# Optimization experiments

Hardware: AMD Instinct MI355X
Metric: run time of the kernel (lower is better)

## Reference

```python
import jax, jax.numpy as jnp
import numpy as np

N, IN_DIM, OUT_DIM, HEADS = 8192, 256, 128, 2


def setup_inputs() -> dict:
    key = jax.random.key(0)
    k1, k2, k3, k4, k5 = jax.random.split(key, 5)
    features = jax.random.normal(k1, (N, IN_DIM), dtype=jnp.float32)
    adjacency = jax.random.randint(k2, (N, N), 0, 2, dtype=jnp.int32)
    # nn.Linear(input_dim, output_dim*heads, bias=False): weight [out, in]
    W = jax.random.normal(k3, (OUT_DIM * HEADS, IN_DIM), dtype=jnp.float32) * 0.05
    attn_src = jax.random.normal(k4, (HEADS, OUT_DIM), dtype=jnp.float32) * 0.05
    attn_dst = jax.random.normal(k5, (HEADS, OUT_DIM), dtype=jnp.float32) * 0.05
    return {"features": features, "adjacency": adjacency, "W": W,
            "attn_src": attn_src, "attn_dst": attn_dst}


def reference(features, adjacency, W, attn_src, attn_dst):
    n = features.shape[0]
    # transformed: [N, H, F]
    transformed = (features @ W.T).reshape(n, HEADS, OUT_DIM)
    src_scores = jnp.einsum('nhf,hf->nh', transformed, attn_src)  # [N, H]
    dst_scores = jnp.einsum('nhf,hf->nh', transformed, attn_dst)  # [N, H]
    # logits: [N_src, N_dst, H]
    logits = jax.nn.leaky_relu(src_scores[:, None, :] + dst_scores[None, :, :],
                               negative_slope=0.2)
    mask = adjacency > 0  # [N, N]
    logits = jnp.where(mask[:, :, None], logits, -jnp.inf)
    attention = jax.nn.softmax(logits, axis=1)  # softmax over dst dim (dim=1)
    attention = jnp.nan_to_num(attention, nan=0.0, posinf=0.0, neginf=0.0)
    aggregated = jnp.einsum('ijh,jhf->ihf', attention, transformed)  # [N, H, F]
    return aggregated.mean(axis=1)  # [N, F]
```

## Files before the change

### kernel.cpp

```cpp
#include <hip/hip_runtime.h>
#include <stdint.h>
#include <stddef.h>

#define NN 8192
#define KD 256
#define CD 256
#define FD 128
#define BI 32
#define BJ 32
#define PACK_BLOCKS 1024

typedef __attribute__((ext_vector_type(4))) float f32x4;
typedef __attribute__((ext_vector_type(8))) short b16x8;

__device__ __forceinline__ unsigned short f2bf(float x) {
    unsigned int u = __float_as_uint(x);
    u += 0x7fffu + ((u >> 16) & 1u);
    return (unsigned short)(u >> 16);
}

__device__ __forceinline__ void async16(const void* g, void* l) {
    __builtin_amdgcn_global_load_lds(
        (const __attribute__((address_space(1))) unsigned int*)g,
        (__attribute__((address_space(3))) unsigned int*)l, 16, 0, 0);
}

__device__ __forceinline__ float exp_pack_store(
    int m8, const float4 d0, const float4 d1, float sv, unsigned short* wdst)
{
    const float dd[8] = {d0.x, d0.y, d0.z, d0.w, d1.x, d1.y, d1.z, d1.w};
    const float ninf = __int_as_float(0xff800000);
    float e[8]; float dp = 0.f;
#pragma unroll
    for (int k = 0; k < 8; ++k) {
        float x = sv + dd[k];
        x = fmaxf(x, 0.f) + 0.2f * fminf(x, 0.f);
        x = (m8 & (1 << k)) ? x : ninf;
        const float ev = __expf(x);
        dp += ev; e[k] = ev;
    }
    union { unsigned short us[8]; b16x8 v; } pk;
#if __has_builtin(__builtin_amdgcn_cvt_pk_bf16_f32)
#pragma unroll
    for (int k = 0; k < 4; ++k) {
        auto p = __builtin_amdgcn_cvt_pk_bf16_f32(e[2 * k], e[2 * k + 1]);
        __builtin_memcpy(&pk.us[2 * k], &p, 4);
    }
#else
#pragma unroll
    for (int k = 0; k < 8; ++k) pk.us[k] = f2bf(e[k]);
#endif
    *(b16x8*)wdst = pk.v;
    return dp;
}

__global__ __launch_bounds__(256) void k_front(
    const float* __restrict__ feat, const float* __restrict__ W,
    const float* __restrict__ asrc, const float* __restrict__ adst,
    const int* __restrict__ adj, unsigned int* __restrict__ mask,
    unsigned short* __restrict__ Tt, float* __restrict__ s_t, float* __restrict__ d_t)
{
    __shared__ unsigned short a_lds[64 * 32];
    __shared__ unsigned short b_lds[256 * 32];
    __shared__ unsigned short tr_lds[256 * 72];
    __shared__ float sc_lds[4][64];
    __shared__ float dc_lds[4][64];

    const int t = threadIdx.x;

    if (blockIdx.x >= 128) {
        const int pb = blockIdx.x - 128;
        const size_t base = (size_t)pb * 16384;
        const int4* a4 = (const int4*)adj;
#pragma unroll 4
        for (int st = 0; st < 64; ++st) {
            const size_t i4 = base + (size_t)st * 256 + t;
            const int4 v = a4[i4];
            unsigned int nib = (v.x != 0 ? 1u : 0u) | (v.y != 0 ? 2u : 0u) |
                               (v.z != 0 ? 4u : 0u) | (v.w != 0 ? 8u : 0u);
            unsigned int wd = nib << (4 * (t & 7));
            wd |= __shfl_xor(wd, 1);
            wd |= __shfl_xor(wd, 2);
            wd |= __shfl_xor(wd, 4);
            if ((t & 7) == 0) mask[i4 >> 3] = wd;
        }
        return;
    }

    const int wave = t >> 6, lane = t & 63;
    const int l15 = lane & 15, quad = lane >> 4;
    const int n0 = blockIdx.x * 64;
    const int ai = t >> 2, ag = t & 3;

    f32x4 acc[4][4] = {};
    for (int kc = 0; kc < 8; ++kc) {
        const int k0 = kc * 32;
        __syncthreads();
        {
            const float* src = feat + (size_t)(n0 + ai) * KD + k0 + ag * 8;
            const float4 v0 = *(const float4*)src;
            const float4 v1 = *(const float4*)(src + 4);
            union { unsigned short us[8]; b16x8 v; } pk;
            pk.us[0] = f2bf(v0.x); pk.us[1] = f2bf(v0.y);
            pk.us[2] = f2bf(v0.z); pk.us[3] = f2bf(v0.w);
            pk.us[4] = f2bf(v1.x); pk.us[5] = f2bf(v1.y);
            pk.us[6] = f2bf(v1.z); pk.us[7] = f2bf(v1.w);
            const int slot = ag ^ ((ai >> 1) & 3);
            *(b16x8*)&a_lds[ai * 32 + slot * 8] = pk.v;
        }
        for (int p = 0; p < 4; ++p) {
            const int G = p * 256 + t;
            const int c = G >> 2, g = G & 3;
            const float* src = W + (size_t)c * KD + k0 + g * 8;
            const float4 v0 = *(const float4*)src;
            const float4 v1 = *(const float4*)(src + 4);
            union { unsigned short us[8]; b16x8 v; } pk;
            pk.us[0] = f2bf(v0.x); pk.us[1] = f2bf(v0.y);
            pk.us[2] = f2bf(v0.z); pk.us[3] = f2bf(v0.w);
            pk.us[4] = f2bf(v1.x); pk.us[5] = f2bf(v1.y);
            pk.us[6] = f2bf(v1.z); pk.us[7] = f2bf(v1.w);
            const int slot = g ^ ((c >> 1) & 3);
            *(b16x8*)&b_lds[c * 32 + slot * 8] = pk.v;
        }
        __syncthreads();
        b16x8 af[4], bfr[4];
        for (int mt = 0; mt < 4; ++mt) {
            const int m = mt * 16 + l15;
            af[mt] = *(const b16x8*)&a_lds[m * 32 + (quad ^ ((m >> 1) & 3)) * 8];
        }
        for (int nt = 0; nt < 4; ++nt) {
            const int c = wave * 64 + nt * 16 + l15;
            bfr[nt] = *(const b16x8*)&b_lds[c * 32 + (quad ^ ((c >> 1) & 3)) * 8];
        }
        for (int mt = 0; mt < 4; ++mt)
            for (int nt = 0; nt < 4; ++nt)
                acc[mt][nt] = __builtin_amdgcn_mfma_f32_16x16x32_bf16(
                    af[mt], bfr[nt], acc[mt][nt], 0, 0, 0);
    }

    float aS[4], aD[4];
    for (int nt = 0; nt < 4; ++nt) {
        const int c = wave * 64 + nt * 16 + l15;
        aS[nt] = asrc[c]; aD[nt] = adst[c];
    }
    for (int mt = 0; mt < 4; ++mt)
        for (int r = 0; r < 4; ++r) {
            float vs = 0.f, vd = 0.f;
            for (int nt = 0; nt < 4; ++nt) {
                const float x = acc[mt][nt][r];
                vs += x * aS[nt]; vd += x * aD[nt];
            }
            vs += __shfl_xor(vs, 1); vd += __shfl_xor(vd, 1);
            vs += __shfl_xor(vs, 2); vd += __shfl_xor(vd, 2);
            vs += __shfl_xor(vs, 4); vd += __shfl_xor(vd, 4);
            vs += __shfl_xor(vs, 8); vd += __shfl_xor(vd, 8);
            if (l15 == 0) {
                const int nl = mt * 16 + quad * 4 + r;
                sc_lds[wave][nl] = vs; dc_lds[wave][nl] = vd;
            }
        }
    for (int mt = 0; mt < 4; ++mt)
        for (int nt = 0; nt < 4; ++nt)
            for (int r = 0; r < 4; ++r) {
                const int c = wave * 64 + nt * 16 + l15;
                const int n = mt * 16 + quad * 4 + r;
                tr_lds[c * 72 + n] = f2bf(acc[mt][nt][r]);
            }
    __syncthreads();
    if (t < 128) {
        const int n = t >> 1, h = t & 1;
        s_t[(size_t)h * NN + n0 + n] = sc_lds[h * 2][n] + sc_lds[h * 2 + 1][n];
        d_t[(size_t)h * NN + n0 + n] = dc_lds[h * 2][n] + dc_lds[h * 2 + 1][n];
    }
    for (int p = 0; p < 8; ++p) {
        const int idx = p * 256 + t;
        const int c = idx >> 3, g = idx & 7;
        *(b16x8*)(Tt + (size_t)c * NN + n0 + g * 8) = *(const b16x8*)&tr_lds[c * 72 + g * 8];
    }
}

__global__ __launch_bounds__(256, 4) void k_gat(
    const unsigned char* __restrict__ maskb, const unsigned short* __restrict__ Tt,
    const float* __restrict__ s_t, const float* __restrict__ d_t,
    float* __restrict__ num_part,
    float* __restrict__ den_part,
    int njt)
{
    __shared__ unsigned short tt_lds[2][256 * 32];
    __shared__ unsigned short w_lds[2][2][32][32];

    const int t = threadIdx.x;
    const int wave = t >> 6, lane = t & 63;
    const int l15 = lane & 15, quad = lane >> 4;
    const int i0 = blockIdx.x * BI;
    const int chunk = blockIdx.y;
    const size_t jbase = (size_t)chunk * njt * BJ;

    const int eh = t >> 7;
    const int wi = (t & 127) >> 2;
    const int g4 = t & 3;
    const int gi = i0 + wi;
    const float sv = s_t[(size_t)eh * NN + gi];
    const int wslot = (g4 ^ ((wi >> 1) & 3)) * 8;

    const int mh = wave >> 1, fh = wave & 1;
    const int cbase = mh * 128 + fh * 64;

    f32x4 acc[2][4] = {};
    float den = 0.f;

    const unsigned char* mrow = maskb + (size_t)gi * (NN / 8) + (jbase >> 3) + g4;
    const float* dp_ = d_t + (size_t)eh * NN + jbase + g4 * 8;

    for (int p = 0; p < 4; ++p) {
        const int G = (p * 4 + wave) * 64 + lane;
        const int c = G >> 2;
        const int g = (G & 3) ^ ((c >> 1) & 3);
        async16(Tt + (size_t)c * NN + jbase + g * 8,
                (char*)&tt_lds[0][0] + (size_t)(p * 4 + wave) * 1024);
    }
    __builtin_amdgcn_sched_barrier(0);
    int cM = mrow[0];
    float4 cD0 = ((const float4*)dp_)[0], cD1 = ((const float4*)dp_)[1];
    {
        const int j1 = (njt > 1) ? 1 : 0;
        int nM = mrow[j1 * 4];
        float4 nD0 = *(const float4*)(dp_ + j1 * BJ);
        float4 nD1 = *(const float4*)(dp_ + j1 * BJ + 4);
        den += exp_pack_store(cM, cD0, cD1, sv, &w_lds[0][eh][wi][wslot]);
        cM = nM; cD0 = nD0; cD1 = nD1;
    }
    asm volatile("s_waitcnt vmcnt(3) lgkmcnt(0)\n\ts_barrier" ::: "memory");

    for (int jt = 0; jt < njt; ++jt) {
        const int cur = jt & 1, nxt = cur ^ 1;
        b16x8 af[2], bfr[4];
        for (int mt = 0; mt < 2; ++mt) {
            const int m = mt * 16 + l15;
            af[mt] = *(const b16x8*)&w_lds[cur][mh][m][(quad ^ ((m >> 1) & 3)) * 8];
        }
        for (int nt = 0; nt < 4; ++nt) {
            const int c = cbase + nt * 16 + l15;
            bfr[nt] = *(const b16x8*)&tt_lds[cur][c * 32 + (quad ^ ((c >> 1) & 3)) * 8];
        }
        const size_t jnext = jbase + (size_t)((jt + 1 < njt) ? jt + 1 : jt) * BJ;
        for (int p = 0; p < 4; ++p) {
            const int G = (p * 4 + wave) * 64 + lane;
            const int c = G >> 2;
            const int g = (G & 3) ^ ((c >> 1) & 3);
            async16(Tt + (size_t)c * NN + jnext + g * 8,
                    (char*)&tt_lds[nxt][0] + (size_t)(p * 4 + wave) * 1024);
        }
        __builtin_amdgcn_sched_barrier(0);
        const int j2 = ((jt + 2 < njt) ? jt + 2 : njt - 1);
        int nM = mrow[j2 * 4];
        float4 nD0 = *(const float4*)(dp_ + j2 * BJ);
        float4 nD1 = *(const float4*)(dp_ + j2 * BJ + 4);
        const float dpv = exp_pack_store(cM, cD0, cD1, sv,
                                         &w_lds[nxt][eh][wi][wslot]);
        if (jt + 1 < njt) den += dpv;
        for (int mt = 0; mt < 2; ++mt)
            for (int nt = 0; nt < 4; ++nt)
                acc[mt][nt] = __builtin_amdgcn_mfma_f32_16x16x32_bf16(
                    af[mt], bfr[nt], acc[mt][nt], 0, 0, 0);
        cM = nM; cD0 = nD0; cD1 = nD1;
        asm volatile("s_waitcnt vmcnt(3) lgkmcnt(0)\n\ts_barrier" ::: "memory");
    }

    float dv = den;
    dv += __shfl_xor(dv, 1); dv += __shfl_xor(dv, 2);
    if (g4 == 0)
        den_part[((size_t)chunk * 2 + eh) * NN + gi] = dv;

    float* np_ = num_part + (size_t)chunk * NN * CD;
    for (int mt = 0; mt < 2; ++mt)
        for (int nt = 0; nt < 4; ++nt)
            for (int r = 0; r < 4; ++r) {
                const int n = i0 + mt * 16 + quad * 4 + r;
                const int c = cbase + nt * 16 + l15;
                np_[(size_t)n * CD + c] = acc[mt][nt][r];
            }
}

__global__ __launch_bounds__(256) void k_combine(
    const float* __restrict__ num_part, const float* __restrict__ den_part,
    float* __restrict__ out, int jsplit)
{
    const int idx = blockIdx.x * 256 + threadIdx.x;
    const int n = idx >> 7, f = idx & 127;
    const size_t row = (size_t)n * CD;
    float n0 = 0.f, n1 = 0.f, d0 = 0.f, d1 = 0.f;
    for (int c = 0; c < jsplit; ++c) {
        const size_t base = (size_t)c * NN * CD;
        n0 += num_part[base + row + f];
        n1 += num_part[base + row + 128 + f];
        d0 += den_part[((size_t)c * 2 + 0) * NN + n];
        d1 += den_part[((size_t)c * 2 + 1) * NN + n];
    }
    const float r0 = d0 != 0.f ? n0 / d0 : 0.f;
    const float r1 = d1 != 0.f ? n1 / d1 : 0.f;
    out[idx] = 0.5f * (r0 + r1);
}

extern "C" void kernel_launch(void* const* d_in, const int* in_sizes, int n_in,
                              void* d_out, int out_size, void* d_ws, size_t ws_size,
                              hipStream_t stream) {
    const float* feat = (const float*)d_in[0];
    const int*   adj  = (const int*)d_in[1];
    const float* W    = (const float*)d_in[2];
    const float* asrc = (const float*)d_in[3];
    const float* adst = (const float*)d_in[4];
    float* out = (float*)d_out;

    const int jsplit = (ws_size >= ((size_t)45 << 20)) ? 4 : 2;
    const int njt = (NN / jsplit) / BJ;

    char* ws = (char*)d_ws;
    unsigned short* Tt = (unsigned short*)ws;
    float* s_t  = (float*)(ws + ((size_t)4 << 20));
    float* d_t  = (float*)(ws + ((size_t)4 << 20) + (64 << 10));
    float* den  = (float*)(ws + ((size_t)4 << 20) + (128 << 10));
    unsigned int* mask = (unsigned int*)(ws + ((size_t)5 << 20));
    float* nump = (float*)(ws + ((size_t)13 << 20));

    k_front<<<128 + PACK_BLOCKS, 256, 0, stream>>>(feat, W, asrc, adst, adj,
                                                   mask, Tt, s_t, d_t);
    k_gat<<<dim3(NN / BI, jsplit), 256, 0, stream>>>((const unsigned char*)mask,
                                                     Tt, s_t, d_t, nump, den, njt);
    k_combine<<<NN * FD / 256, 256, 0, stream>>>(nump, den, out, jsplit);
}
```

Before: 506.2 us.

## Drop LDS staging in GAT kernel; compute attention fragments directly in registers

The GAT aggregation kernel no longer stages the transformed features and attention weights through double-buffered LDS. Each wave now handles one head and 32 rows, computes its exp/bf16 attention fragment straight into MFMA A-operand registers, and loads the B fragments directly from global memory. Block tile grows to 64 rows, with per-wave accumulators doubled to 2x8 tiles and occupancy hint lowered to 3. This removes LDS traffic and barriers, but gives up software prefetch. Each global load of Tt is also shared by fewer rows per wave, so more global and L2 traffic is expected.

```diff
diff --git a/kernel.cpp b/kernel.cpp
--- a/kernel.cpp
+++ b/kernel.cpp
@@ -6,8 +6,6 @@
 #define KD 256
 #define CD 256
 #define FD 128
-#define BI 32
-#define BJ 32
 #define PACK_BLOCKS 1024
 
 typedef __attribute__((ext_vector_type(4))) float f32x4;
@@ -19,14 +17,8 @@
     return (unsigned short)(u >> 16);
 }
 
-__device__ __forceinline__ void async16(const void* g, void* l) {
-    __builtin_amdgcn_global_load_lds(
-        (const __attribute__((address_space(1))) unsigned int*)g,
-        (__attribute__((address_space(3))) unsigned int*)l, 16, 0, 0);
-}
-
-__device__ __forceinline__ float exp_pack_store(
-    int m8, const float4 d0, const float4 d1, float sv, unsigned short* wdst)
+__device__ __forceinline__ float exp_frag(
+    int m8, const float4 d0, const float4 d1, float sv, b16x8* frag)
 {
     const float dd[8] = {d0.x, d0.y, d0.z, d0.w, d1.x, d1.y, d1.z, d1.w};
     const float ninf = __int_as_float(0xff800000);
@@ -50,7 +42,7 @@
 #pragma unroll
     for (int k = 0; k < 8; ++k) pk.us[k] = f2bf(e[k]);
 #endif
-    *(b16x8*)wdst = pk.v;
+    *frag = pk.v;
     return dp;
 }
 
@@ -179,105 +171,73 @@
     }
 }
 
-__global__ __launch_bounds__(256, 4) void k_gat(
+__global__ __launch_bounds__(256, 3) void k_gat(
     const unsigned char* __restrict__ maskb, const unsigned short* __restrict__ Tt,
     const float* __restrict__ s_t, const float* __restrict__ d_t,
     float* __restrict__ num_part,
     float* __restrict__ den_part,
     int njt)
 {
-    __shared__ unsigned short tt_lds[2][256 * 32];
-    __shared__ unsigned short w_lds[2][2][32][32];
-
     const int t = threadIdx.x;
     const int wave = t >> 6, lane = t & 63;
     const int l15 = lane & 15, quad = lane >> 4;
-    const int i0 = blockIdx.x * BI;
+    const int h = wave >> 1, ih = wave & 1;
+    const int i0 = blockIdx.x * 64 + ih * 32;
     const int chunk = blockIdx.y;
-    const size_t jbase = (size_t)chunk * njt * BJ;
-
-    const int eh = t >> 7;
-    const int wi = (t & 127) >> 2;
-    const int g4 = t & 3;
-    const int gi = i0 + wi;
-    const float sv = s_t[(size_t)eh * NN + gi];
-    const int wslot = (g4 ^ ((wi >> 1) & 3)) * 8;
-
-    const int mh = wave >> 1, fh = wave & 1;
-    const int cbase = mh * 128 + fh * 64;
-
-    f32x4 acc[2][4] = {};
-    float den = 0.f;
-
-    const unsigned char* mrow = maskb + (size_t)gi * (NN / 8) + (jbase >> 3) + g4;
-    const float* dp_ = d_t + (size_t)eh * NN + jbase + g4 * 8;
-
-    for (int p = 0; p < 4; ++p) {
-        const int G = (p * 4 + wave) * 64 + lane;
-        const int c = G >> 2;
-        const int g = (G & 3) ^ ((c >> 1) & 3);
-        async16(Tt + (size_t)c * NN + jbase + g * 8,
-                (char*)&tt_lds[0][0] + (size_t)(p * 4 + wave) * 1024);
-    }
-    __builtin_amdgcn_sched_barrier(0);
-    int cM = mrow[0];
-    float4 cD0 = ((const float4*)dp_)[0], cD1 = ((const float4*)dp_)[1];
-    {
-        const int j1 = (njt > 1) ? 1 : 0;
-        int nM = mrow[j1 * 4];
-        float4 nD0 = *(const float4*)(dp_ + j1 * BJ);
-        float4 nD1 = *(const float4*)(dp_ + j1 * BJ + 4);
-        den += exp_pack_store(cM, cD0, cD1, sv, &w_lds[0][eh][wi][wslot]);
-        cM = nM; cD0 = nD0; cD1 = nD1;
-    }
-    asm volatile("s_waitcnt vmcnt(3) lgkmcnt(0)\n\ts_barrier" ::: "memory");
+    const size_t jbase = (size_t)chunk * njt * 32;
+
+    const int r0 = i0 + l15;
+    const int r1 = i0 + 16 + l15;
+    const float sv0 = s_t[(size_t)h * NN + r0];
+    const float sv1 = s_t[(size_t)h * NN + r1];
+
+    const unsigned char* m0 = maskb + (size_t)r0 * (NN / 8) + (jbase >> 3) + quad;
+    const unsigned char* m1 = maskb + (size_t)r1 * (NN / 8) + (jbase >> 3) + quad;
+    const float* dp = d_t + (size_t)h * NN + jbase + quad * 8;
+    const unsigned short* tb = Tt + (size_t)(h * 128 + l15) * NN + jbase + quad * 8;
+
+    f32x4 acc[2][8] = {};
+    float den0 = 0.f, den1 = 0.f;
 
     for (int jt = 0; jt < njt; ++jt) {
-        const int cur = jt & 1, nxt = cur ^ 1;
-        b16x8 af[2], bfr[4];
-        for (int mt = 0; mt < 2; ++mt) {
-            const int m = mt * 16 + l15;
-            af[mt] = *(const b16x8*)&w_lds[cur][mh][m][(quad ^ ((m >> 1) & 3)) * 8];
-        }
-        for (int nt = 0; nt < 4; ++nt) {
-            const int c = cbase + nt * 16 + l15;
-            bfr[nt] = *(const b16x8*)&tt_lds[cur][c * 32 + (quad ^ ((c >> 1) & 3)) * 8];
-        }
-        const size_t jnext = jbase + (size_t)((jt + 1 < njt) ? jt + 1 : jt) * BJ;
-        for (int p = 0; p < 4; ++p) {
-            const int G = (p * 4 + wave) * 64 + lane;
-            const int c = G >> 2;
-            const int g = (G & 3) ^ ((c >> 1) & 3);
-            async16(Tt + (size_t)c * NN + jnext + g * 8,
-                    (char*)&tt_lds[nxt][0] + (size_t)(p * 4 + wave) * 1024);
-        }
-        __builtin_amdgcn_sched_barrier(0);
-        const int j2 = ((jt + 2 < njt) ? jt + 2 : njt - 1);
-        int nM = mrow[j2 * 4];
-        float4 nD0 = *(const float4*)(dp_ + j2 * BJ);
-        float4 nD1 = *(const float4*)(dp_ + j2 * BJ + 4);
-        const float dpv = exp_pack_store(cM, cD0, cD1, sv,
-                                         &w_lds[nxt][eh][wi][wslot]);
-        if (jt + 1 < njt) den += dpv;
-        for (int mt = 0; mt < 2; ++mt)
-            for (int nt = 0; nt < 4; ++nt)
-                acc[mt][nt] = __builtin_amdgcn_mfma_f32_16x16x32_bf16(
-                    af[mt], bfr[nt], acc[mt][nt], 0, 0, 0);
-        cM = nM; cD0 = nD0; cD1 = nD1;
-        asm volatile("s_waitcnt vmcnt(3) lgkmcnt(0)\n\ts_barrier" ::: "memory");
-    }
-
-    float dv = den;
-    dv += __shfl_xor(dv, 1); dv += __shfl_xor(dv, 2);
-    if (g4 == 0)
-        den_part[((size_t)chunk * 2 + eh) * NN + gi] = dv;
+        const int jo = jt * 32;
+        const int mb0 = m0[jt * 4];
+        const int mb1 = m1[jt * 4];
+        const float4 dv0 = *(const float4*)(dp + jo);
+        const float4 dv1 = *(const float4*)(dp + jo + 4);
+        b16x8 bfr[8];
+#pragma unroll
+        for (int nt = 0; nt < 8; ++nt)
+            bfr[nt] = *(const b16x8*)(tb + (size_t)nt * 16 * NN + jo);
+        b16x8 a0, a1;
+        den0 += exp_frag(mb0, dv0, dv1, sv0, &a0);
+        den1 += exp_frag(mb1, dv0, dv1, sv1, &a1);
+#pragma unroll
+        for (int nt = 0; nt < 8; ++nt)
+            acc[0][nt] = __builtin_amdgcn_mfma_f32_16x16x32_bf16(
+                a0, bfr[nt], acc[0][nt], 0, 0, 0);
+#pragma unroll
+        for (int nt = 0; nt < 8; ++nt)
+            acc[1][nt] = __builtin_amdgcn_mfma_f32_16x16x32_bf16(
+                a1, bfr[nt], acc[1][nt], 0, 0, 0);
+    }
+
+    den0 += __shfl_xor(den0, 16); den0 += __shfl_xor(den0, 32);
+    den1 += __shfl_xor(den1, 16); den1 += __shfl_xor(den1, 32);
+    if (quad == 0) {
+        den_part[((size_t)chunk * 2 + h) * NN + r0] = den0;
+        den_part[((size_t)chunk * 2 + h) * NN + r1] = den1;
+    }
 
     float* np_ = num_part + (size_t)chunk * NN * CD;
+#pragma unroll
     for (int mt = 0; mt < 2; ++mt)
-        for (int nt = 0; nt < 4; ++nt)
+#pragma unroll
+        for (int nt = 0; nt < 8; ++nt)
+#pragma unroll
             for (int r = 0; r < 4; ++r) {
                 const int n = i0 + mt * 16 + quad * 4 + r;
-                const int c = cbase + nt * 16 + l15;
+                const int c = h * 128 + nt * 16 + l15;
                 np_[(size_t)n * CD + c] = acc[mt][nt][r];
             }
 }
@@ -313,7 +273,7 @@
     float* out = (float*)d_out;
 
     const int jsplit = (ws_size >= ((size_t)45 << 20)) ? 4 : 2;
-    const int njt = (NN / jsplit) / BJ;
+    const int njt = (NN / jsplit) / 32;
 
     char* ws = (char*)d_ws;
     unsigned short* Tt = (unsigned short*)ws;
@@ -325,7 +285,7 @@
 
     k_front<<<128 + PACK_BLOCKS, 256, 0, stream>>>(feat, W, asrc, adst, adj,
                                                    mask, Tt, s_t, d_t);
-    k_gat<<<dim3(NN / BI, jsplit), 256, 0, stream>>>((const unsigned char*)mask,
+    k_gat<<<dim3(NN / 64, jsplit), 256, 0, stream>>>((const unsigned char*)mask,
                                                      Tt, s_t, d_t, nump, den, njt);
     k_combine<<<NN * FD / 256, 256, 0, stream>>>(nump, den, out, jsplit);
 }
```

Measured after the change: 565.8 us. +11.8%, slower.

## Factor exp of leaky-relu into precomputed per-node exponentials and tile mask/T layouts

Applied to the files above, without the earlier changes.

Replaces the per-edge exp(leaky_relu(s+d)) with max(exp(s)exp(d), exp(0.2s)exp(0.2d)), using four per-node exponential arrays computed in the front kernel. This removes the transcendental from the inner loop, leaving two multiplies and a max per edge. The mask is repacked into a 32-row tiled transposed layout and the transformed features into contiguous 32-column blocks, so each tile load hits one contiguous region. Skipping max-subtraction risks overflow for large scores, and the inner loop now issues more global loads per tile.

```diff
diff --git a/kernel.cpp b/kernel.cpp
--- a/kernel.cpp
+++ b/kernel.cpp
@@ -8,7 +8,7 @@
 #define FD 128
 #define BI 32
 #define BJ 32
-#define PACK_BLOCKS 1024
+#define PACK_BLOCKS 512
 
 typedef __attribute__((ext_vector_type(4))) float f32x4;
 typedef __attribute__((ext_vector_type(8))) short b16x8;
@@ -25,19 +25,18 @@
         (__attribute__((address_space(3))) unsigned int*)l, 16, 0, 0);
 }
 
-__device__ __forceinline__ float exp_pack_store(
-    int m8, const float4 d0, const float4 d1, float sv, unsigned short* wdst)
+__device__ __forceinline__ float wsel_store(
+    int m8, const float4 f0, const float4 f1, const float4 h0, const float4 h1,
+    float Ei, float Gi, unsigned short* wdst)
 {
-    const float dd[8] = {d0.x, d0.y, d0.z, d0.w, d1.x, d1.y, d1.z, d1.w};
-    const float ninf = __int_as_float(0xff800000);
+    const float ff[8] = {f0.x, f0.y, f0.z, f0.w, f1.x, f1.y, f1.z, f1.w};
+    const float hh[8] = {h0.x, h0.y, h0.z, h0.w, h1.x, h1.y, h1.z, h1.w};
     float e[8]; float dp = 0.f;
 #pragma unroll
     for (int k = 0; k < 8; ++k) {
-        float x = sv + dd[k];
-        x = fmaxf(x, 0.f) + 0.2f * fminf(x, 0.f);
-        x = (m8 & (1 << k)) ? x : ninf;
-        const float ev = __expf(x);
-        dp += ev; e[k] = ev;
+        float w = fmaxf(Ei * ff[k], Gi * hh[k]);
+        w = (m8 & (1 << k)) ? w : 0.f;
+        dp += w; e[k] = w;
     }
     union { unsigned short us[8]; b16x8 v; } pk;
 #if __has_builtin(__builtin_amdgcn_cvt_pk_bf16_f32)
@@ -57,32 +56,44 @@
 __global__ __launch_bounds__(256) void k_front(
     const float* __restrict__ feat, const float* __restrict__ W,
     const float* __restrict__ asrc, const float* __restrict__ adst,
-    const int* __restrict__ adj, unsigned int* __restrict__ mask,
-    unsigned short* __restrict__ Tt, float* __restrict__ s_t, float* __restrict__ d_t)
+    const int* __restrict__ adj, unsigned char* __restrict__ MT,
+    unsigned short* __restrict__ TB,
+    float* __restrict__ SE, float* __restrict__ SG,
+    float* __restrict__ SF, float* __restrict__ SH)
 {
     __shared__ unsigned short a_lds[64 * 32];
     __shared__ unsigned short b_lds[256 * 32];
     __shared__ unsigned short tr_lds[256 * 72];
     __shared__ float sc_lds[4][64];
     __shared__ float dc_lds[4][64];
+    __shared__ unsigned char pk_lds[1024 * 16];
 
     const int t = threadIdx.x;
 
     if (blockIdx.x >= 128) {
         const int pb = blockIdx.x - 128;
-        const size_t base = (size_t)pb * 16384;
+        const int I = pb >> 1, half = pb & 1;
+        const int row_base = I * 32 + half * 16;
         const int4* a4 = (const int4*)adj;
 #pragma unroll 4
-        for (int st = 0; st < 64; ++st) {
-            const size_t i4 = base + (size_t)st * 256 + t;
-            const int4 v = a4[i4];
+        for (int st = 0; st < 128; ++st) {
+            const int g = st * 256 + t;
+            const int row16 = g >> 11;
+            const int j4 = g & 2047;
+            const int4 v = a4[(size_t)(row_base + row16) * 2048 + j4];
             unsigned int nib = (v.x != 0 ? 1u : 0u) | (v.y != 0 ? 2u : 0u) |
                                (v.z != 0 ? 4u : 0u) | (v.w != 0 ? 8u : 0u);
-            unsigned int wd = nib << (4 * (t & 7));
-            wd |= __shfl_xor(wd, 1);
-            wd |= __shfl_xor(wd, 2);
-            wd |= __shfl_xor(wd, 4);
-            if ((t & 7) == 0) mask[i4 >> 3] = wd;
+            unsigned int b = nib << (4 * (t & 1));
+            b |= __shfl_xor(b, 1);
+            if ((t & 1) == 0) pk_lds[(j4 >> 1) * 16 + row16] = (unsigned char)b;
+        }
+        __syncthreads();
+        unsigned int* mt32 = (unsigned int*)MT;
+        const unsigned int* src = (const unsigned int*)pk_lds;
+        for (int i = 0; i < 16; ++i) {
+            const int w = i * 256 + t;
+            const int jb = w >> 2, r4 = w & 3;
+            mt32[(size_t)I * 8192 + jb * 8 + half * 4 + r4] = src[w];
         }
         return;
     }
@@ -169,19 +180,26 @@
     __syncthreads();
     if (t < 128) {
         const int n = t >> 1, h = t & 1;
-        s_t[(size_t)h * NN + n0 + n] = sc_lds[h * 2][n] + sc_lds[h * 2 + 1][n];
-        d_t[(size_t)h * NN + n0 + n] = dc_lds[h * 2][n] + dc_lds[h * 2 + 1][n];
+        const float s = sc_lds[h * 2][n] + sc_lds[h * 2 + 1][n];
+        const float d = dc_lds[h * 2][n] + dc_lds[h * 2 + 1][n];
+        SE[(size_t)h * NN + n0 + n] = __expf(s);
+        SG[(size_t)h * NN + n0 + n] = __expf(0.2f * s);
+        SF[(size_t)h * NN + n0 + n] = __expf(d);
+        SH[(size_t)h * NN + n0 + n] = __expf(0.2f * d);
     }
     for (int p = 0; p < 8; ++p) {
         const int idx = p * 256 + t;
         const int c = idx >> 3, g = idx & 7;
-        *(b16x8*)(Tt + (size_t)c * NN + n0 + g * 8) = *(const b16x8*)&tr_lds[c * 72 + g * 8];
+        unsigned short* dst = TB + ((size_t)((n0 >> 5) + (g >> 2))) * 8192
+                              + c * 32 + (g & 3) * 8;
+        *(b16x8*)dst = *(const b16x8*)&tr_lds[c * 72 + g * 8];
     }
 }
 
 __global__ __launch_bounds__(256, 4) void k_gat(
-    const unsigned char* __restrict__ maskb, const unsigned short* __restrict__ Tt,
-    const float* __restrict__ s_t, const float* __restrict__ d_t,
+    const unsigned char* __restrict__ MT, const unsigned short* __restrict__ TB,
+    const float* __restrict__ SE, const float* __restrict__ SG,
+    const float* __restrict__ SF, const float* __restrict__ SH,
     float* __restrict__ num_part,
     float* __restrict__ den_part,
     int njt)
@@ -197,74 +215,81 @@
     const size_t jbase = (size_t)chunk * njt * BJ;
 
     const int eh = t >> 7;
-    const int wi = (t & 127) >> 2;
+    const int wi = (t >> 2) & 31;
     const int g4 = t & 3;
     const int gi = i0 + wi;
-    const float sv = s_t[(size_t)eh * NN + gi];
-    const int wslot = (g4 ^ ((wi >> 1) & 3)) * 8;
+    const float Ei = SE[(size_t)eh * NN + gi];
+    const float Gi = SG[(size_t)eh * NN + gi];
+    const int wslot = (g4 ^ (wi & 3) ^ ((wi >> 2) & 3)) * 8;
 
     const int mh = wave >> 1, fh = wave & 1;
-    const int cbase = mh * 128 + fh * 64;
+    const int cb = mh * 128 + fh * 64;
 
     f32x4 acc[2][4] = {};
     float den = 0.f;
 
-    const unsigned char* mrow = maskb + (size_t)gi * (NN / 8) + (jbase >> 3) + g4;
-    const float* dp_ = d_t + (size_t)eh * NN + jbase + g4 * 8;
+    const unsigned short* tb0 = TB + (jbase >> 5) * 8192;
+    const unsigned char* mrow = MT + ((size_t)(i0 >> 5)) * 32768
+                                + (jbase >> 3) * 32 + g4 * 32 + wi;
+    const float* fp = SF + (size_t)eh * NN + jbase + g4 * 8;
+    const float* hp = SH + (size_t)eh * NN + jbase + g4 * 8;
 
     for (int p = 0; p < 4; ++p) {
         const int G = (p * 4 + wave) * 64 + lane;
         const int c = G >> 2;
         const int g = (G & 3) ^ ((c >> 1) & 3);
-        async16(Tt + (size_t)c * NN + jbase + g * 8,
+        async16(tb0 + (size_t)c * 32 + g * 8,
                 (char*)&tt_lds[0][0] + (size_t)(p * 4 + wave) * 1024);
     }
     __builtin_amdgcn_sched_barrier(0);
     int cM = mrow[0];
-    float4 cD0 = ((const float4*)dp_)[0], cD1 = ((const float4*)dp_)[1];
+    float4 cF0 = *(const float4*)(fp),     cF1 = *(const float4*)(fp + 4);
+    float4 cH0 = *(const float4*)(hp),     cH1 = *(const float4*)(hp + 4);
+    int nM; float4 nF0, nF1, nH0, nH1;
     {
         const int j1 = (njt > 1) ? 1 : 0;
-        int nM = mrow[j1 * 4];
-        float4 nD0 = *(const float4*)(dp_ + j1 * BJ);
-        float4 nD1 = *(const float4*)(dp_ + j1 * BJ + 4);
-        den += exp_pack_store(cM, cD0, cD1, sv, &w_lds[0][eh][wi][wslot]);
-        cM = nM; cD0 = nD0; cD1 = nD1;
-    }
-    asm volatile("s_waitcnt vmcnt(3) lgkmcnt(0)\n\ts_barrier" ::: "memory");
+        nM = mrow[j1 * 128];
+        nF0 = *(const float4*)(fp + j1 * BJ); nF1 = *(const float4*)(fp + j1 * BJ + 4);
+        nH0 = *(const float4*)(hp + j1 * BJ); nH1 = *(const float4*)(hp + j1 * BJ + 4);
+        den += wsel_store(cM, cF0, cF1, cH0, cH1, Ei, Gi, &w_lds[0][eh][wi][wslot]);
+        cM = nM; cF0 = nF0; cF1 = nF1; cH0 = nH0; cH1 = nH1;
+    }
+    asm volatile("s_waitcnt vmcnt(5) lgkmcnt(0)\n\ts_barrier" ::: "memory");
 
     for (int jt = 0; jt < njt; ++jt) {
         const int cur = jt & 1, nxt = cur ^ 1;
         b16x8 af[2], bfr[4];
         for (int mt = 0; mt < 2; ++mt) {
             const int m = mt * 16 + l15;
-            af[mt] = *(const b16x8*)&w_lds[cur][mh][m][(quad ^ ((m >> 1) & 3)) * 8];
+            af[mt] = *(const b16x8*)
+                &w_lds[cur][mh][m][(quad ^ (m & 3) ^ ((m >> 2) & 3)) * 8];
         }
         for (int nt = 0; nt < 4; ++nt) {
-            const int c = cbase + nt * 16 + l15;
+            const int c = cb + nt * 16 + l15;
             bfr[nt] = *(const b16x8*)&tt_lds[cur][c * 32 + (quad ^ ((c >> 1) & 3)) * 8];
         }
-        const size_t jnext = jbase + (size_t)((jt + 1 < njt) ? jt + 1 : jt) * BJ;
+        const unsigned short* tbn = tb0 + (size_t)((jt + 1 < njt) ? jt + 1 : jt) * 8192;
         for (int p = 0; p < 4; ++p) {
             const int G = (p * 4 + wave) * 64 + lane;
             const int c = G >> 2;
             const int g = (G & 3) ^ ((c >> 1) & 3);
-            async16(Tt + (size_t)c * NN + jnext + g * 8,
+            async16(tbn + (size_t)c * 32 + g * 8,
                     (char*)&tt_lds[nxt][0] + (size_t)(p * 4 + wave) * 1024);
         }
         __builtin_amdgcn_sched_barrier(0);
-        const int j2 = ((jt + 2 < njt) ? jt + 2 : njt - 1);
-        int nM = mrow[j2 * 4];
-        float4 nD0 = *(const float4*)(dp_ + j2 * BJ);
-        float4 nD1 = *(const float4*)(dp_ + j2 * BJ + 4);
-        const float dpv = exp_pack_store(cM, cD0, cD1, sv,
-                                         &w_lds[nxt][eh][wi][wslot]);
+        const int j2 = (jt + 2 < njt) ? jt + 2 : njt - 1;
+        nM = mrow[j2 * 128];
+        nF0 = *(const float4*)(fp + j2 * BJ); nF1 = *(const float4*)(fp + j2 * BJ + 4);
+        nH0 = *(const float4*)(hp + j2 * BJ); nH1 = *(const float4*)(hp + j2 * BJ + 4);
+        const float dpv = wsel_store(cM, cF0, cF1, cH0, cH1, Ei, Gi,
+                                     &w_lds[nxt][eh][wi][wslot]);
         if (jt + 1 < njt) den += dpv;
         for (int mt = 0; mt < 2; ++mt)
             for (int nt = 0; nt < 4; ++nt)
                 acc[mt][nt] = __builtin_amdgcn_mfma_f32_16x16x32_bf16(
                     af[mt], bfr[nt], acc[mt][nt], 0, 0, 0);
-        cM = nM; cD0 = nD0; cD1 = nD1;
-        asm volatile("s_waitcnt vmcnt(3) lgkmcnt(0)\n\ts_barrier" ::: "memory");
+        cM = nM; cF0 = nF0; cF1 = nF1; cH0 = nH0; cH1 = nH1;
+        asm volatile("s_waitcnt vmcnt(5) lgkmcnt(0)\n\ts_barrier" ::: "memory");
     }
 
     float dv = den;
@@ -277,7 +302,7 @@
         for (int nt = 0; nt < 4; ++nt)
             for (int r = 0; r < 4; ++r) {
                 const int n = i0 + mt * 16 + quad * 4 + r;
-                const int c = cbase + nt * 16 + l15;
+                const int c = cb + nt * 16 + l15;
                 np_[(size_t)n * CD + c] = acc[mt][nt][r];
             }
 }
@@ -316,16 +341,18 @@
     const int njt = (NN / jsplit) / BJ;
 
     char* ws = (char*)d_ws;
-    unsigned short* Tt = (unsigned short*)ws;
-    float* s_t  = (float*)(ws + ((size_t)4 << 20));
-    float* d_t  = (float*)(ws + ((size_t)4 << 20) + (64 << 10));
-    float* den  = (float*)(ws + ((size_t)4 << 20) + (128 << 10));
-    unsigned int* mask = (unsigned int*)(ws + ((size_t)5 << 20));
+    unsigned short* TB = (unsigned short*)ws;
+    float* SE = (float*)(ws + ((size_t)4 << 20));
+    float* SG = (float*)(ws + ((size_t)4 << 20) + (64 << 10));
+    float* SF = (float*)(ws + ((size_t)4 << 20) + (128 << 10));
+    float* SH = (float*)(ws + ((size_t)4 << 20) + (192 << 10));
+    float* den = (float*)(ws + ((size_t)4 << 20) + (256 << 10));
+    unsigned char* MT = (unsigned char*)(ws + ((size_t)5 << 20));
     float* nump = (float*)(ws + ((size_t)13 << 20));
 
     k_front<<<128 + PACK_BLOCKS, 256, 0, stream>>>(feat, W, asrc, adst, adj,
-                                                   mask, Tt, s_t, d_t);
-    k_gat<<<dim3(NN / BI, jsplit), 256, 0, stream>>>((const unsigned char*)mask,
-                                                     Tt, s_t, d_t, nump, den, njt);
+                                                   MT, TB, SE, SG, SF, SH);
+    k_gat<<<dim3(NN / BI, jsplit), 256, 0, stream>>>(MT, TB, SE, SG, SF, SH,
+                                                     nump, den, njt);
     k_combine<<<NN * FD / 256, 256, 0, stream>>>(nump, den, out, jsplit);
 }
```

After: 502.1 us. About the same (-0.8%).
